# Performance work log

Measured on AMD Instinct MI355X. Metric: run time of the kernel, lower is better.

## Reference

```python
import jax, jax.numpy as jnp
import numpy as np

B, N, EN, EE = 2, 384, 128, 64
H, FN, FE = 8, 32, 32          # num_heads, out_node_features, out_edge_features
F = FN * H                     # projected dim = 256 (node and edge proj dims must match: shared attention_linear)


def setup_inputs() -> dict:
    key = jax.random.key(0)
    ks = jax.random.split(key, 8)
    s = lambda k, shape, fan_in: jax.random.normal(k, shape, jnp.float32) / np.sqrt(fan_in)
    return {
        "nodes": jax.random.normal(ks[0], (B, N, EN), jnp.float32),
        "edges": jax.random.normal(ks[1], (B, N, N, EE), jnp.float32),
        "node_mask": jnp.ones((B, N), dtype=bool),
        "W_node": s(ks[2], (EN, F), EN),
        "b_node": jnp.zeros((F,), jnp.float32),
        "W_edge": s(ks[3], (EE, F), EE),
        "b_edge": jnp.zeros((F,), jnp.float32),
        "W_att": s(ks[4], (F, H), F),
    }


def reference(nodes, edges, node_mask, W_node, b_node, W_edge, b_edge, W_att):
    # Dense projections (deterministic=True -> dropout is identity)
    nf = nodes @ W_node + b_node                      # [b,n,F]
    ef = edges @ W_edge + b_edge                      # [b,n,n,F]

    q = nf @ W_att                                    # [b,n,H]
    s_nodes = jnp.einsum('bik,bjk->bij', q, q) / jnp.sqrt(jnp.float32(FN))
    eq = ef @ W_att                                   # [b,n,n,H]
    s_edges = jnp.einsum('bik,bijk->bij', q, eq) / jnp.sqrt(jnp.float32(FE))

    m = node_mask[..., None].astype(nf.dtype)         # [b,n,1] -- masks rows i (faithful to source)
    aw_n = jax.nn.softmax(s_nodes * m, axis=-1)       # [b,n,n]
    aw_e = jax.nn.softmax(s_edges * m, axis=-1)       # [b,n,n]

    attn_w_nodes = jnp.einsum('bij,bik->bjk', aw_n, nf)       # [b,n,F]
    attn_w_edges = aw_e[..., None] * ef                        # [b,n,n,F]
    agg_edge = jnp.einsum('bij,bijk->bik', aw_e, ef)           # [b,n,F]

    updated_nodes = nf + attn_w_nodes + agg_edge               # [b,n,F]

    agg_node = jnp.einsum('bij,bik->bijk', aw_n, nf)           # [b,n,n,F] outer product
    updated_edges = ef + attn_w_edges + agg_node               # [b,n,n,F]

    re = jax.nn.elu(updated_edges)
    re = (re + jnp.swapaxes(re, 1, 2)) / 2
    return jax.nn.elu(updated_nodes), re
```

## Files before the change

kernel.cpp:

```cpp
#include <hip/hip_runtime.h>
#include <cmath>

#define NB 2
#define NN 384
#define EN 128
#define EE 64
#define NH 8
#define FF 256
#define NT 24
#define NPAIRS 300

typedef float f32x4 __attribute__((ext_vector_type(4)));
typedef __bf16 bf16x8 __attribute__((ext_vector_type(8)));

union AB { uint4 u; bf16x8 v; unsigned short s[8]; };

__device__ __forceinline__ float b2f(unsigned short u) {
  union { unsigned int i; float f; } x; x.i = ((unsigned int)u) << 16; return x.f;
}
__device__ __forceinline__ unsigned short f2b(float f) {
  union { float f; unsigned int i; } x; x.f = f;
  unsigned int r = (x.i + 0x7fffu + ((x.i >> 16) & 1u)) >> 16;
  return (unsigned short)r;
}
__device__ __forceinline__ float elu1(float x) { return x > 0.f ? x : expm1f(x); }

__device__ __forceinline__ bf16x8 load8_cvt(const float* p) {
  float4 x = *(const float4*)p;
  float4 y = *(const float4*)(p + 4);
  AB u;
  u.s[0] = f2b(x.x); u.s[1] = f2b(x.y); u.s[2] = f2b(x.z); u.s[3] = f2b(x.w);
  u.s[4] = f2b(y.x); u.s[5] = f2b(y.y); u.s[6] = f2b(y.z); u.s[7] = f2b(y.w);
  return u.v;
}

__device__ __forceinline__ float block_max(float v, float* red) {
#pragma unroll
  for (int o = 32; o > 0; o >>= 1) v = fmaxf(v, __shfl_down(v, o));
  if ((threadIdx.x & 63) == 0) red[threadIdx.x >> 6] = v;
  __syncthreads();
  v = fmaxf(fmaxf(red[0], red[1]), fmaxf(red[2], red[3]));
  __syncthreads();
  return v;
}
__device__ __forceinline__ float block_sum(float v, float* red) {
#pragma unroll
  for (int o = 32; o > 0; o >>= 1) v += __shfl_down(v, o);
  if ((threadIdx.x & 63) == 0) red[threadIdx.x >> 6] = v;
  __syncthreads();
  v = red[0] + red[1] + red[2] + red[3];
  __syncthreads();
  return v;
}

__global__ __launch_bounds__(256) void k1_proj(
    const float* __restrict__ nodes, const float* __restrict__ W_node,
    const float* __restrict__ b_node, const float* __restrict__ W_att,
    float* __restrict__ nf, float* __restrict__ q)
{
  __shared__ float nd[EN];
  __shared__ float nfrow[FF];
  int bi = blockIdx.x;
  int tid = threadIdx.x;
  const float* nrow = nodes + (size_t)bi * EN;
  if (tid < EN) nd[tid] = nrow[tid];
  __syncthreads();
  float acc = b_node[tid];
#pragma unroll 4
  for (int c = 0; c < EN; ++c) acc += nd[c] * W_node[c * FF + tid];
  nfrow[tid] = acc;
  nf[(size_t)bi * FF + tid] = acc;
  __syncthreads();
  if (tid < NH) {
    float qa = 0.f;
#pragma unroll 4
    for (int f = 0; f < FF; ++f) qa += nfrow[f] * W_att[f * NH + tid];
    q[bi * NH + tid] = qa;
  }
}

__global__ __launch_bounds__(256) void k2_scores(
    const float* __restrict__ edges, const float* __restrict__ W_edge,
    const float* __restrict__ b_edge, const float* __restrict__ W_att,
    const float* __restrict__ qg, float* __restrict__ awn, float* __restrict__ awe,
    float* __restrict__ wsum)
{
  __shared__ float qL[NN * NH];
  __shared__ __align__(16) unsigned short eL[NN * 72];
  __shared__ float tL[FF];
  __shared__ float vL[EE + 1];
  __shared__ float snL[NN], seL[NN];
  __shared__ float red[4];

  int bi = blockIdx.x;
  int b = bi / NN, i = bi % NN;
  int tid = threadIdx.x;

  for (int idx = tid; idx < NN * NH; idx += 256) qL[idx] = qg[b * NN * NH + idx];
  const float* erow = edges + ((size_t)b * NN + i) * NN * EE;
  for (int v = tid; v < NN * EE / 4; v += 256) {
    int j = v >> 4, c4 = v & 15;
    float4 d = *(const float4*)(erow + j * EE + c4 * 4);
    ushort4 s;
    s.x = f2b(d.x); s.y = f2b(d.y); s.z = f2b(d.z); s.w = f2b(d.w);
    *(ushort4*)&eL[j * 72 + c4 * 4] = s;
  }
  __syncthreads();

  float qi[NH];
#pragma unroll
  for (int h = 0; h < NH; ++h) qi[h] = qL[i * NH + h];

  {
    float a = 0.f;
#pragma unroll
    for (int h = 0; h < NH; ++h) a += qi[h] * W_att[tid * NH + h];
    tL[tid] = a;
  }
  __syncthreads();
  if (tid < EE) {
    float a = 0.f;
#pragma unroll 4
    for (int f = 0; f < FF; ++f) a += W_edge[tid * FF + f] * tL[f];
    vL[tid] = a;
  } else if (tid == EE) {
    float a = 0.f;
    for (int f = 0; f < FF; ++f) a += b_edge[f] * tL[f];
    vL[EE] = a;
  }
  __syncthreads();

  const float rs = 0.17677669529663687f;
  for (int j = tid; j < NN; j += 256) {
    float se = vL[EE];
#pragma unroll
    for (int c8 = 0; c8 < 8; ++c8) {
      AB u; u.u = *(const uint4*)&eL[j * 72 + c8 * 8];
#pragma unroll
      for (int k = 0; k < 8; ++k) se += vL[c8 * 8 + k] * b2f(u.s[k]);
    }
    float sn = 0.f;
#pragma unroll
    for (int h = 0; h < NH; ++h) sn += qi[h] * qL[j * NH + h];
    snL[j] = sn * rs;
    seL[j] = se * rs;
  }
  __syncthreads();

  float mn = -1e30f, me = -1e30f;
  for (int j = tid; j < NN; j += 256) { mn = fmaxf(mn, snL[j]); me = fmaxf(me, seL[j]); }
  mn = block_max(mn, red);
  me = block_max(me, red);
  float ssn = 0.f, sse = 0.f;
  for (int j = tid; j < NN; j += 256) {
    float en = expf(snL[j] - mn); snL[j] = en; ssn += en;
    float ee2 = expf(seL[j] - me); seL[j] = ee2; sse += ee2;
  }
  ssn = block_sum(ssn, red);
  sse = block_sum(sse, red);
  float in_ = 1.f / ssn, ie_ = 1.f / sse;
  float* awnRow = awn + ((size_t)b * NN + i) * NN;
  float* aweRow = awe + ((size_t)b * NN + i) * NN;
  for (int j = tid; j < NN; j += 256) {
    awnRow[j] = snL[j] * in_;
    float ae = seL[j] * ie_;
    aweRow[j] = ae;
    seL[j] = ae;
  }
  __syncthreads();
  if (tid < EE) {
    float a = 0.f;
    for (int j = 0; j < NN; ++j) a += seL[j] * b2f(eL[j * 72 + tid]);
    wsum[((size_t)b * NN + i) * EE + tid] = a;
  }
}

__global__ __launch_bounds__(256) void k3_nodes(
    const float* __restrict__ nf, const float* __restrict__ awn,
    const float* __restrict__ wsum, const float* __restrict__ W_edge,
    const float* __restrict__ b_edge, float* __restrict__ out0)
{
  __shared__ float awT[256];
  __shared__ float wsT[16 * EE];
  int b = blockIdx.x / NT, t = blockIdx.x % NT;
  int i0 = t * 16;
  int f = threadIdx.x;
  float acc[16];
#pragma unroll
  for (int ii = 0; ii < 16; ++ii) acc[ii] = 0.f;

  for (int c0 = 0; c0 < NN; c0 += 16) {
    __syncthreads();
    { int r = f >> 4, ii = f & 15;
      awT[f] = awn[((size_t)(b * NN + c0 + r)) * NN + i0 + ii]; }
    __syncthreads();
    for (int r = 0; r < 16; ++r) {
      float nfv = nf[((size_t)(b * NN + c0 + r)) * FF + f];
#pragma unroll
      for (int ii = 0; ii < 16; ++ii) acc[ii] += awT[r * 16 + ii] * nfv;
    }
  }
  __syncthreads();
  for (int idx = f; idx < 16 * EE; idx += 256) wsT[idx] = wsum[((size_t)(b * NN + i0)) * EE + idx];
  __syncthreads();
  for (int c = 0; c < EE; ++c) {
    float wev = W_edge[c * FF + f];
#pragma unroll
    for (int ii = 0; ii < 16; ++ii) acc[ii] += wsT[ii * EE + c] * wev;
  }
  float bev = b_edge[f];
#pragma unroll
  for (int ii = 0; ii < 16; ++ii) {
    float tot = acc[ii] + bev + nf[((size_t)(b * NN + i0 + ii)) * FF + f];
    out0[((size_t)(b * NN + i0 + ii)) * FF + f] = elu1(tot);
  }
}

__global__ __launch_bounds__(1024) void k4_edges(
    const float* __restrict__ edges, const float* __restrict__ nf,
    const float* __restrict__ awn, const float* __restrict__ awe,
    const float* __restrict__ W_edge, const float* __restrict__ b_edge,
    float* __restrict__ out1)
{
  __shared__ __align__(16) unsigned short WeT[FF * 72];
  __shared__ float nfA[16 * FF];
  __shared__ float nfB[16 * FF];
  __shared__ float aw1n[256], aw1e[256], aw2n[256], aw2e[256];
  __shared__ float beL[FF];
  __shared__ __align__(16) unsigned short re2buf[16 * 1176];

  int blk = blockIdx.x;
  int b = blk / NPAIRS;
  int p = blk % NPAIRS;
  int ti = 0, rowlen = NT;
  while (p >= rowlen) { p -= rowlen; rowlen--; ti++; }
  int tj = ti + p;
  int i0 = ti * 16, j0 = tj * 16;
  int tid = threadIdx.x;

  for (int idx = tid; idx < EE * FF; idx += 1024) {
    int n = idx & 255, k = idx >> 8;
    WeT[n * 72 + k] = f2b(W_edge[k * FF + n]);
  }
  for (int idx = tid; idx < 16 * FF; idx += 1024) {
    int r = idx >> 8, f = idx & 255;
    nfA[idx] = nf[((size_t)(b * NN + i0 + r)) * FF + f];
    nfB[idx] = nf[((size_t)(b * NN + j0 + r)) * FF + f];
  }
  if (tid < 256) {
    int r = tid >> 4, c = tid & 15;
    aw1n[tid] = awn[((size_t)(b * NN + i0 + r)) * NN + j0 + c];
    aw1e[tid] = awe[((size_t)(b * NN + i0 + r)) * NN + j0 + c];
    aw2n[tid] = awn[((size_t)(b * NN + j0 + r)) * NN + i0 + c];
    aw2e[tid] = awe[((size_t)(b * NN + j0 + r)) * NN + i0 + c];
  } else if (tid < 512) {
    beL[tid - 256] = b_edge[tid - 256];
  }

  int w = tid >> 6, lane = tid & 63, q = lane >> 4, ln = lane & 15;
  const float* e1 = edges + ((size_t)(b * NN + i0 + w) * NN + (j0 + ln)) * EE;
  const float* e2 = edges + ((size_t)(b * NN + j0 + w) * NN + (i0 + ln)) * EE;
  bf16x8 a1[2], a2[2];
  a1[0] = load8_cvt(e1 + q * 8);
  a1[1] = load8_cvt(e1 + 32 + q * 8);
  a2[0] = load8_cvt(e2 + q * 8);
  a2[1] = load8_cvt(e2 + 32 + q * 8);
  __syncthreads();

  float* outT = out1 + (size_t)b * NN * NN * FF;
  const int awb = w * 16;

  for (int fc = 0; fc < 4; ++fc) {
    f32x4 acc2[4];
#pragma unroll
    for (int t = 0; t < 4; ++t) acc2[t] = (f32x4){0.f, 0.f, 0.f, 0.f};
#pragma unroll
    for (int t = 0; t < 4; ++t) {
      int n = fc * 64 + t * 16 + ln;
      bf16x8 b0 = *(const bf16x8*)&WeT[n * 72 + q * 8];
      bf16x8 b1 = *(const bf16x8*)&WeT[n * 72 + 32 + q * 8];
      acc2[t] = __builtin_amdgcn_mfma_f32_16x16x32_bf16(a2[0], b0, acc2[t], 0, 0, 0);
      acc2[t] = __builtin_amdgcn_mfma_f32_16x16x32_bf16(a2[1], b1, acc2[t], 0, 0, 0);
    }
#pragma unroll
    for (int t = 0; t < 4; ++t) {
      int fl = t * 16 + ln, fg = fc * 64 + fl;
      float nfv = nfB[w * FF + fg], bev = beL[fg];
#pragma unroll
      for (int r = 0; r < 4; ++r) {
        int m = q * 4 + r;
        float ef = acc2[t][r] + bev;
        float ue = (1.f + aw2e[awb + m]) * ef + aw2n[awb + m] * nfv;
        re2buf[w * 1176 + m * 72 + fl] = f2b(elu1(ue));
      }
    }
    __syncthreads();

    f32x4 acc1[4];
#pragma unroll
    for (int t = 0; t < 4; ++t) acc1[t] = (f32x4){0.f, 0.f, 0.f, 0.f};
#pragma unroll
    for (int t = 0; t < 4; ++t) {
      int n = fc * 64 + t * 16 + ln;
      bf16x8 b0 = *(const bf16x8*)&WeT[n * 72 + q * 8];
      bf16x8 b1 = *(const bf16x8*)&WeT[n * 72 + 32 + q * 8];
      acc1[t] = __builtin_amdgcn_mfma_f32_16x16x32_bf16(a1[0], b0, acc1[t], 0, 0, 0);
      acc1[t] = __builtin_amdgcn_mfma_f32_16x16x32_bf16(a1[1], b1, acc1[t], 0, 0, 0);
    }
    float vals[4][4];
#pragma unroll
    for (int t = 0; t < 4; ++t) {
      int fl = t * 16 + ln, fg = fc * 64 + fl;
      float nfv = nfA[w * FF + fg], bev = beL[fg];
#pragma unroll
      for (int r = 0; r < 4; ++r) {
        int m = q * 4 + r;
        float ef = acc1[t][r] + bev;
        float ue = (1.f + aw1e[awb + m]) * ef + aw1n[awb + m] * nfv;
        float re1 = elu1(ue);
        float re2 = b2f(re2buf[m * 1176 + w * 72 + fl]);
        vals[t][r] = 0.5f * (re1 + re2);
      }
    }
    __syncthreads();
#pragma unroll
    for (int t = 0; t < 4; ++t)
#pragma unroll
      for (int r = 0; r < 4; ++r)
        re2buf[w * 1176 + (q * 4 + r) * 72 + t * 16 + ln] = f2b(vals[t][r]);
    __syncthreads();

    for (int v = tid; v < 2048; v += 1024) {
      int f8 = v & 7, bb = (v >> 3) & 15, a = v >> 7;
      AB u; u.u = *(const uint4*)&re2buf[a * 1176 + bb * 72 + f8 * 8];
      float4 lo, hi;
      lo.x = b2f(u.s[0]); lo.y = b2f(u.s[1]); lo.z = b2f(u.s[2]); lo.w = b2f(u.s[3]);
      hi.x = b2f(u.s[4]); hi.y = b2f(u.s[5]); hi.z = b2f(u.s[6]); hi.w = b2f(u.s[7]);
      float* dst = outT + ((size_t)(i0 + a) * NN + (j0 + bb)) * FF + fc * 64 + f8 * 8;
      *(float4*)dst = lo;
      *(float4*)(dst + 4) = hi;
      if (ti != tj) {
        float* dst2 = outT + ((size_t)(j0 + bb) * NN + (i0 + a)) * FF + fc * 64 + f8 * 8;
        *(float4*)dst2 = lo;
        *(float4*)(dst2 + 4) = hi;
      }
    }
    __syncthreads();
  }
}

extern "C" void kernel_launch(void* const* d_in, const int* in_sizes, int n_in,
                              void* d_out, int out_size, void* d_ws, size_t ws_size,
                              hipStream_t stream)
{
  const float* nodes  = (const float*)d_in[0];
  const float* edges  = (const float*)d_in[1];
  const float* W_node = (const float*)d_in[3];
  const float* b_node = (const float*)d_in[4];
  const float* W_edge = (const float*)d_in[5];
  const float* b_edge = (const float*)d_in[6];
  const float* W_att  = (const float*)d_in[7];

  float* ws   = (float*)d_ws;
  float* nf   = ws;
  float* q    = ws + 196608;
  float* awn  = ws + 202752;
  float* awe  = ws + 497664;
  float* wsum = ws + 792576;

  float* out0 = (float*)d_out;
  float* out1 = out0 + (size_t)NB * NN * FF;

  hipLaunchKernelGGL(k1_proj,   dim3(NB * NN),     dim3(256),  0, stream,
                     nodes, W_node, b_node, W_att, nf, q);
  hipLaunchKernelGGL(k2_scores, dim3(NB * NN),     dim3(256),  0, stream,
                     edges, W_edge, b_edge, W_att, q, awn, awe, wsum);
  hipLaunchKernelGGL(k3_nodes,  dim3(NB * NT),     dim3(256),  0, stream,
                     nf, awn, wsum, W_edge, b_edge, out0);
  hipLaunchKernelGGL(k4_edges,  dim3(NB * NPAIRS), dim3(1024), 0, stream,
                     edges, nf, awn, awe, W_edge, b_edge, out1);
}
```

Before: 557.3 us.

## Parallelize small reductions, shrink node tiles, and store edge outputs directly

The node projection and score kernels now split their serial dot-product reductions across all threads, with partial sums combined in shared memory. The node-output kernel uses tiles of 4 rows instead of 16, which launches more blocks. Exact exp and expm1 are replaced with the fast __expf. The edge kernel drops its second shared-memory staging pass and bf16 repacking, and each lane writes its fp32 results straight to both the direct and the transposed output locations. That removes barriers and a round-trip through shared memory, but the stores become narrow scalar writes and the transposed ones are strided, which may hurt write coalescing on the dominant output stream.

```diff
diff --git a/kernel.cpp b/kernel.cpp
--- a/kernel.cpp
+++ b/kernel.cpp
@@ -9,6 +9,8 @@
 #define FF 256
 #define NT 24
 #define NPAIRS 300
+#define K3R 4
+#define K3T (NN / K3R)
 
 typedef float f32x4 __attribute__((ext_vector_type(4)));
 typedef __bf16 bf16x8 __attribute__((ext_vector_type(8)));
@@ -23,7 +25,9 @@
   unsigned int r = (x.i + 0x7fffu + ((x.i >> 16) & 1u)) >> 16;
   return (unsigned short)r;
 }
-__device__ __forceinline__ float elu1(float x) { return x > 0.f ? x : expm1f(x); }
+__device__ __forceinline__ float elu_fast(float x) {
+  return x > 0.f ? x : __expf(x) - 1.f;
+}
 
 __device__ __forceinline__ bf16x8 load8_cvt(const float* p) {
   float4 x = *(const float4*)p;
@@ -60,6 +64,7 @@
 {
   __shared__ float nd[EN];
   __shared__ float nfrow[FF];
+  __shared__ float qpart[32][NH];
   int bi = blockIdx.x;
   int tid = threadIdx.x;
   const float* nrow = nodes + (size_t)bi * EN;
@@ -71,11 +76,22 @@
   nfrow[tid] = acc;
   nf[(size_t)bi * FF + tid] = acc;
   __syncthreads();
+  {
+    int h = tid & 7, part = tid >> 3;
+    float qa = 0.f;
+#pragma unroll
+    for (int k = 0; k < 8; ++k) {
+      int f = part * 8 + k;
+      qa += nfrow[f] * W_att[f * NH + h];
+    }
+    qpart[part][h] = qa;
+  }
+  __syncthreads();
   if (tid < NH) {
-    float qa = 0.f;
-#pragma unroll 4
-    for (int f = 0; f < FF; ++f) qa += nfrow[f] * W_att[f * NH + tid];
-    q[bi * NH + tid] = qa;
+    float s = 0.f;
+#pragma unroll
+    for (int p = 0; p < 32; ++p) s += qpart[p][tid];
+    q[bi * NH + tid] = s;
   }
 }
 
@@ -88,7 +104,8 @@
   __shared__ float qL[NN * NH];
   __shared__ __align__(16) unsigned short eL[NN * 72];
   __shared__ float tL[FF];
-  __shared__ float vL[EE + 1];
+  __shared__ float vL[EE];
+  __shared__ float part4[4][EE];
   __shared__ float snL[NN], seL[NN];
   __shared__ float red[4];
 
@@ -117,22 +134,24 @@
     for (int h = 0; h < NH; ++h) a += qi[h] * W_att[tid * NH + h];
     tL[tid] = a;
   }
-  __syncthreads();
-  if (tid < EE) {
+  float bconst = block_sum(b_edge[tid] * tL[tid], red);
+
+  {
+    int c = tid & 63, part = tid >> 6;
+    const float* wrow = W_edge + (size_t)c * FF + part * 64;
+    const float* trow = tL + part * 64;
     float a = 0.f;
-#pragma unroll 4
-    for (int f = 0; f < FF; ++f) a += W_edge[tid * FF + f] * tL[f];
-    vL[tid] = a;
-  } else if (tid == EE) {
-    float a = 0.f;
-    for (int f = 0; f < FF; ++f) a += b_edge[f] * tL[f];
-    vL[EE] = a;
-  }
+#pragma unroll 8
+    for (int k = 0; k < 64; ++k) a += wrow[k] * trow[k];
+    part4[part][c] = a;
+  }
+  __syncthreads();
+  if (tid < EE) vL[tid] = part4[0][tid] + part4[1][tid] + part4[2][tid] + part4[3][tid];
   __syncthreads();
 
   const float rs = 0.17677669529663687f;
   for (int j = tid; j < NN; j += 256) {
-    float se = vL[EE];
+    float se = bconst;
 #pragma unroll
     for (int c8 = 0; c8 < 8; ++c8) {
       AB u; u.u = *(const uint4*)&eL[j * 72 + c8 * 8];
@@ -153,8 +172,8 @@
   me = block_max(me, red);
   float ssn = 0.f, sse = 0.f;
   for (int j = tid; j < NN; j += 256) {
-    float en = expf(snL[j] - mn); snL[j] = en; ssn += en;
-    float ee2 = expf(seL[j] - me); seL[j] = ee2; sse += ee2;
+    float en = __expf(snL[j] - mn); snL[j] = en; ssn += en;
+    float ee2 = __expf(seL[j] - me); seL[j] = ee2; sse += ee2;
   }
   ssn = block_sum(ssn, red);
   sse = block_sum(sse, red);
@@ -168,11 +187,16 @@
     seL[j] = ae;
   }
   __syncthreads();
-  if (tid < EE) {
+  {
+    int c = tid & 63, part = tid >> 6;
     float a = 0.f;
-    for (int j = 0; j < NN; ++j) a += seL[j] * b2f(eL[j * 72 + tid]);
-    wsum[((size_t)b * NN + i) * EE + tid] = a;
-  }
+    for (int j = part * 96; j < part * 96 + 96; ++j) a += seL[j] * b2f(eL[j * 72 + c]);
+    part4[part][c] = a;
+  }
+  __syncthreads();
+  if (tid < EE)
+    wsum[((size_t)b * NN + i) * EE + tid] =
+        part4[0][tid] + part4[1][tid] + part4[2][tid] + part4[3][tid];
 }
 
 __global__ __launch_bounds__(256) void k3_nodes(
@@ -180,39 +204,42 @@
     const float* __restrict__ wsum, const float* __restrict__ W_edge,
     const float* __restrict__ b_edge, float* __restrict__ out0)
 {
-  __shared__ float awT[256];
-  __shared__ float wsT[16 * EE];
-  int b = blockIdx.x / NT, t = blockIdx.x % NT;
-  int i0 = t * 16;
+  __shared__ float awT[16 * K3R];
+  __shared__ float wsT[K3R * EE];
+  int b = blockIdx.x / K3T, t = blockIdx.x % K3T;
+  int i0 = t * K3R;
   int f = threadIdx.x;
-  float acc[16];
-#pragma unroll
-  for (int ii = 0; ii < 16; ++ii) acc[ii] = 0.f;
+  float acc[K3R];
+#pragma unroll
+  for (int ii = 0; ii < K3R; ++ii) acc[ii] = 0.f;
 
   for (int c0 = 0; c0 < NN; c0 += 16) {
     __syncthreads();
-    { int r = f >> 4, ii = f & 15;
-      awT[f] = awn[((size_t)(b * NN + c0 + r)) * NN + i0 + ii]; }
+    if (f < 16 * K3R) {
+      int r = f >> 2, ii = f & 3;
+      awT[f] = awn[((size_t)(b * NN + c0 + r)) * NN + i0 + ii];
+    }
     __syncthreads();
+#pragma unroll
     for (int r = 0; r < 16; ++r) {
       float nfv = nf[((size_t)(b * NN + c0 + r)) * FF + f];
 #pragma unroll
-      for (int ii = 0; ii < 16; ++ii) acc[ii] += awT[r * 16 + ii] * nfv;
-    }
-  }
-  __syncthreads();
-  for (int idx = f; idx < 16 * EE; idx += 256) wsT[idx] = wsum[((size_t)(b * NN + i0)) * EE + idx];
+      for (int ii = 0; ii < K3R; ++ii) acc[ii] += awT[r * K3R + ii] * nfv;
+    }
+  }
+  __syncthreads();
+  wsT[f] = wsum[((size_t)(b * NN + i0)) * EE + f];
   __syncthreads();
   for (int c = 0; c < EE; ++c) {
     float wev = W_edge[c * FF + f];
 #pragma unroll
-    for (int ii = 0; ii < 16; ++ii) acc[ii] += wsT[ii * EE + c] * wev;
+    for (int ii = 0; ii < K3R; ++ii) acc[ii] += wsT[ii * EE + c] * wev;
   }
   float bev = b_edge[f];
 #pragma unroll
-  for (int ii = 0; ii < 16; ++ii) {
+  for (int ii = 0; ii < K3R; ++ii) {
     float tot = acc[ii] + bev + nf[((size_t)(b * NN + i0 + ii)) * FF + f];
-    out0[((size_t)(b * NN + i0 + ii)) * FF + f] = elu1(tot);
+    out0[((size_t)(b * NN + i0 + ii)) * FF + f] = elu_fast(tot);
   }
 }
 
@@ -227,7 +254,7 @@
   __shared__ float nfB[16 * FF];
   __shared__ float aw1n[256], aw1e[256], aw2n[256], aw2e[256];
   __shared__ float beL[FF];
-  __shared__ __align__(16) unsigned short re2buf[16 * 1176];
+  __shared__ unsigned short exbuf[16 * 1176];
 
   int blk = blockIdx.x;
   int b = blk / NPAIRS;
@@ -269,6 +296,8 @@
 
   float* outT = out1 + (size_t)b * NN * NN * FF;
   const int awb = w * 16;
+  const size_t row1base = ((size_t)(i0 + w) * NN + j0) * FF;
+  const size_t row2base = ((size_t)j0 * NN + (i0 + w)) * FF;
 
   for (int fc = 0; fc < 4; ++fc) {
     f32x4 acc2[4];
@@ -291,7 +320,7 @@
         int m = q * 4 + r;
         float ef = acc2[t][r] + bev;
         float ue = (1.f + aw2e[awb + m]) * ef + aw2n[awb + m] * nfv;
-        re2buf[w * 1176 + m * 72 + fl] = f2b(elu1(ue));
+        exbuf[w * 1176 + m * 73 + fl] = f2b(elu_fast(ue));
       }
     }
     __syncthreads();
@@ -307,7 +336,6 @@
       acc1[t] = __builtin_amdgcn_mfma_f32_16x16x32_bf16(a1[0], b0, acc1[t], 0, 0, 0);
       acc1[t] = __builtin_amdgcn_mfma_f32_16x16x32_bf16(a1[1], b1, acc1[t], 0, 0, 0);
     }
-    float vals[4][4];
 #pragma unroll
     for (int t = 0; t < 4; ++t) {
       int fl = t * 16 + ln, fg = fc * 64 + fl;
@@ -317,32 +345,12 @@
         int m = q * 4 + r;
         float ef = acc1[t][r] + bev;
         float ue = (1.f + aw1e[awb + m]) * ef + aw1n[awb + m] * nfv;
-        float re1 = elu1(ue);
-        float re2 = b2f(re2buf[m * 1176 + w * 72 + fl]);
-        vals[t][r] = 0.5f * (re1 + re2);
-      }
-    }
-    __syncthreads();
-#pragma unroll
-    for (int t = 0; t < 4; ++t)
-#pragma unroll
-      for (int r = 0; r < 4; ++r)
-        re2buf[w * 1176 + (q * 4 + r) * 72 + t * 16 + ln] = f2b(vals[t][r]);
-    __syncthreads();
-
-    for (int v = tid; v < 2048; v += 1024) {
-      int f8 = v & 7, bb = (v >> 3) & 15, a = v >> 7;
-      AB u; u.u = *(const uint4*)&re2buf[a * 1176 + bb * 72 + f8 * 8];
-      float4 lo, hi;
-      lo.x = b2f(u.s[0]); lo.y = b2f(u.s[1]); lo.z = b2f(u.s[2]); lo.w = b2f(u.s[3]);
-      hi.x = b2f(u.s[4]); hi.y = b2f(u.s[5]); hi.z = b2f(u.s[6]); hi.w = b2f(u.s[7]);
-      float* dst = outT + ((size_t)(i0 + a) * NN + (j0 + bb)) * FF + fc * 64 + f8 * 8;
-      *(float4*)dst = lo;
-      *(float4*)(dst + 4) = hi;
-      if (ti != tj) {
-        float* dst2 = outT + ((size_t)(j0 + bb) * NN + (i0 + a)) * FF + fc * 64 + f8 * 8;
-        *(float4*)dst2 = lo;
-        *(float4*)(dst2 + 4) = hi;
+        float re1 = elu_fast(ue);
+        float re2 = b2f(exbuf[m * 1176 + w * 73 + fl]);
+        float val = 0.5f * (re1 + re2);
+        outT[row1base + (size_t)m * FF + fg] = val;
+        if (ti != tj)
+          outT[row2base + (size_t)m * NN * FF + fg] = val;
       }
     }
     __syncthreads();
@@ -375,7 +383,7 @@
                      nodes, W_node, b_node, W_att, nf, q);
   hipLaunchKernelGGL(k2_scores, dim3(NB * NN),     dim3(256),  0, stream,
                      edges, W_edge, b_edge, W_att, q, awn, awe, wsum);
-  hipLaunchKernelGGL(k3_nodes,  dim3(NB * NT),     dim3(256),  0, stream,
+  hipLaunchKernelGGL(k3_nodes,  dim3(NB * K3T),    dim3(256),  0, stream,
                      nf, awn, wsum, W_edge, b_edge, out0);
   hipLaunchKernelGGL(k4_edges,  dim3(NB * NPAIRS), dim3(1024), 0, stream,
                      edges, nf, awn, awe, W_edge, b_edge, out1);
```

After: 471.6 us. -15.4%, faster.
